# Optimization experiments

Measured on AMD Instinct MI355X. Metric: run time of the kernel, lower is better.

The kernel has to match this reference:

```python
import jax, jax.numpy as jnp
import numpy as np
import math

NUM_HEADS = 8
WINDOW = 8  # stage=1


def _windowed_attention(q, kv, Wq, bq, Wk, bk, Wv, bv, Wo, bo):
    B, N, C = q.shape
    H = W = int(math.isqrt(N))
    nh, ws = NUM_HEADS, WINDOW
    hd = C // nh
    scale = hd ** -0.5

    qp = q @ Wq + bq   # (B, N, C)
    kp = kv @ Wk + bk
    vp = kv @ Wv + bv

    def to_windows(x):
        # (B, N, C) -> (B, nh, nWh*nWw, ws*ws, hd)
        x = x.reshape(B, H // ws, ws, W // ws, ws, nh, hd)
        x = x.transpose(0, 5, 1, 3, 2, 4, 6)  # B, nh, nWh, nWw, ws, ws, hd
        return x.reshape(B, nh, (H // ws) * (W // ws), ws * ws, hd)

    qw = to_windows(qp)
    kw = to_windows(kp)
    vw = to_windows(vp)

    attn = jnp.einsum('bhnqd,bhnkd->bhnqk', qw, kw) * scale
    attn = jax.nn.softmax(attn.astype(jnp.float32), axis=-1).astype(qw.dtype)
    ow = jnp.einsum('bhnqk,bhnkd->bhnqd', attn, vw)

    # window reverse: (B, nh, nW, ws*ws, hd) -> (B, N, C)
    ow = ow.reshape(B, nh, H // ws, W // ws, ws, ws, hd)
    ow = ow.transpose(0, 2, 4, 3, 5, 1, 6)  # B, nWh, ws, nWw, ws, nh, hd
    x = ow.reshape(B, N, C)

    return x @ Wo + bo


def setup_inputs() -> dict:
    key = jax.random.key(0)
    ks = jax.random.split(key, 7)
    B, N, C = 4, 16384, 256
    s = 1.0 / math.sqrt(C)
    return {
        'q': jax.random.normal(ks[0], (B, N, C), jnp.float32),
        'kv': jax.random.normal(ks[1], (B, N, C), jnp.float32),
        'Wq': jax.random.normal(ks[2], (C, C), jnp.float32) * s,
        'bq': jnp.zeros((C,), jnp.float32),
        'Wk': jax.random.normal(ks[3], (C, C), jnp.float32) * s,
        'bk': jnp.zeros((C,), jnp.float32),
        'Wv': jax.random.normal(ks[4], (C, C), jnp.float32) * s,
        'bv': jnp.zeros((C,), jnp.float32),
        'Wo': jax.random.normal(ks[5], (C, C), jnp.float32) * s,
        'bo': jnp.zeros((C,), jnp.float32),
    }


def reference(q, kv, Wq, bq, Wk, bk, Wv, bv, Wo, bo):
    return _windowed_attention(q, kv, Wq, bq, Wk, bk, Wv, bv, Wo, bo)
```

## Files before the change

### kernel.cpp

```cpp
#include <hip/hip_runtime.h>
#include <hip/hip_bf16.h>

typedef __bf16 bf16;
typedef __bf16 bf16x8 __attribute__((ext_vector_type(8)));
typedef __bf16 bf16x4 __attribute__((ext_vector_type(4)));
typedef float  f32x4  __attribute__((ext_vector_type(4)));

#define DEVINL __device__ __forceinline__

DEVINL void gll16(const void* g, void* l) {
  __builtin_amdgcn_global_load_lds(
      (const __attribute__((address_space(1))) unsigned int*)g,
      (__attribute__((address_space(3))) unsigned int*)l, 16, 0, 0);
}

__global__ void k_prep(const float* __restrict__ Wq, const float* __restrict__ Wk,
                       const float* __restrict__ Wv, const float* __restrict__ Wo,
                       bf16* __restrict__ packQ, bf16* __restrict__ packO) {
  const int n = threadIdx.x;
  const int k = blockIdx.x;
  const int m = blockIdx.y;
  const int kk = k & 63, iter4 = k >> 6;
  const int h = kk >> 5, kg = (kk >> 3) & 3, e = k & 7;
  if (m < 3) {
    const float* W = (m == 0) ? Wq : (m == 1) ? Wk : Wv;
    const bf16 v = (bf16)W[k * 256 + n];
    const int nglob = m * 256 + n;
    const int tile = nglob >> 7, row = nglob & 127;
    const int kgs = kg ^ ((row >> 1) & 3);
    packQ[(size_t)((tile * 4 + iter4) * 1024 + h * 512 + row * 4 + kgs) * 8 + e] = v;
  } else {
    const float w = Wo[k * 256 + n];
    const bf16 hi = (bf16)w;
    const bf16 v = (m == 3) ? hi : (bf16)(w - (float)hi);
    const int iter = (m - 3) * 4 + iter4;
    const int tile = n >> 7, row = n & 127;
    const int kgs = kg ^ ((row >> 1) & 3);
    packO[(size_t)((tile * 8 + iter) * 1024 + h * 512 + row * 4 + kgs) * 8 + e] = v;
  }
}

__global__ __launch_bounds__(256, 3) void k_qkv(
    const float* __restrict__ q, const float* __restrict__ kv,
    const bf16* __restrict__ packQ,
    const float* __restrict__ bq, const float* __restrict__ bk,
    const float* __restrict__ bvv,
    bf16* __restrict__ qp, bf16* __restrict__ kp, bf16* __restrict__ vp) {
  __shared__ __align__(16) bf16 Bs[2][2][128 * 32];
  __shared__ __align__(16) bf16 Alds[128 * 64];

  const int g = blockIdx.x, xcd = g & 7, s = g >> 3;
  const int nb = s % 6, mh = s / 6;
  const int m0 = (mh * 8 + xcd) * 128;
  const float* A = (nb < 2) ? q : kv;

  const int tid = threadIdx.x, lane = tid & 63, wave = tid >> 6;
  const int lm = lane & 15, lq = lane >> 4;
  const int swzlq = lq ^ ((lm >> 1) & 3);
  const int mw = wave * 32;

  f32x4 acc[2][8];
#pragma unroll
  for (int t = 0; t < 2; ++t)
#pragma unroll
    for (int nf = 0; nf < 8; ++nf) acc[t][nf] = (f32x4)0.0f;

  const bf16* pbase = packQ + (size_t)nb * 4 * 8192;

  const int arow = tid >> 4;
  const int ac16 = tid & 15;
  float4 ar[8];

  auto loadA = [&](int it) {
#pragma unroll
    for (int u = 0; u < 8; ++u) {
      const int row = u * 16 + arow;
      ar[u] = *(const float4*)(A + (size_t)(m0 + row) * 256 + it * 64 + ac16 * 4);
    }
  };
  auto writeA = [&]() {
    const int gsl = ac16 >> 1, half = ac16 & 1;
#pragma unroll
    for (int u = 0; u < 8; ++u) {
      const int row = u * 16 + arow;
      const float4 f = ar[u];
      bf16x4 v;
      v[0] = (bf16)f.x; v[1] = (bf16)f.y; v[2] = (bf16)f.z; v[3] = (bf16)f.w;
      *(bf16x4*)&Alds[row * 64 + ((gsl ^ (row & 7)) << 3) + half * 4] = v;
    }
  };
  auto stageB = [&](int it, int buf) {
    const bf16* pit = pbase + it * 8192;
#pragma unroll
    for (int u = 0; u < 4; ++u) {
      const int c = u * 256 + tid;
      bf16* dst = (u < 2) ? &Bs[buf][0][c * 8] : &Bs[buf][1][(c - 512) * 8];
      gll16(pit + c * 8, dst);
    }
  };

  loadA(0);
  writeA();
  stageB(0, 0);
  __syncthreads();

#pragma unroll
  for (int i = 0; i < 4; ++i) {
    const int cur = i & 1;
    if (i < 3) {
      stageB(i + 1, cur ^ 1);
      loadA(i + 1);
    }
#pragma unroll
    for (int ks = 0; ks < 2; ++ks) {
      bf16x8 av[2], bvf[8];
#pragma unroll
      for (int t = 0; t < 2; ++t) {
        const int row = mw + t * 16 + lm;
        av[t] = *(const bf16x8*)&Alds[row * 64 + (((ks * 4 + lq) ^ (lm & 7)) << 3)];
      }
#pragma unroll
      for (int nf = 0; nf < 8; ++nf)
        bvf[nf] = *(const bf16x8*)&Bs[cur][ks][(nf * 16 + lm) * 32 + swzlq * 8];
#pragma unroll
      for (int t = 0; t < 2; ++t)
#pragma unroll
        for (int nf = 0; nf < 8; ++nf)
          acc[t][nf] = __builtin_amdgcn_mfma_f32_16x16x32_bf16(av[t], bvf[nf], acc[t][nf], 0, 0, 0);
    }
    if (i < 3) {
      __syncthreads();
      writeA();
      __syncthreads();
    }
  }

  const int ncbase = (nb * 128) & 255;
  bf16* op = (nb < 2) ? qp : (nb < 4) ? kp : vp;
  const float* bp = (nb < 2) ? bq : (nb < 4) ? bk : bvv;
#pragma unroll
  for (int t = 0; t < 2; ++t)
#pragma unroll
    for (int nf = 0; nf < 8; ++nf) {
      const int nc = ncbase + nf * 16 + lm;
      const float bval = bp[nc];
#pragma unroll
      for (int r = 0; r < 4; ++r) {
        const int mg = m0 + mw + t * 16 + lq * 4 + r;
        op[(size_t)mg * 256 + nc] = (bf16)(acc[t][nf][r] + bval);
      }
    }
}

__global__ __launch_bounds__(256, 3) void k_oproj(
    const bf16* __restrict__ ao, const bf16* __restrict__ packO,
    const float* __restrict__ bo, float* __restrict__ out) {
  __shared__ __align__(16) bf16 Bs[2][2][128 * 32];
  __shared__ __align__(16) bf16 Alds[128 * 64];

  const int g = blockIdx.x, xcd = g & 7, s = g >> 3;
  const int nb = s & 1, mh = s >> 1;
  const int m0 = (mh * 8 + xcd) * 128;

  const int tid = threadIdx.x, lane = tid & 63, wave = tid >> 6;
  const int lm = lane & 15, lq = lane >> 4;
  const int swzlq = lq ^ ((lm >> 1) & 3);
  const int mw = wave * 32;

  f32x4 acc[2][8];
#pragma unroll
  for (int t = 0; t < 2; ++t)
#pragma unroll
    for (int nf = 0; nf < 8; ++nf) acc[t][nf] = (f32x4)0.0f;

  const bf16* pbase = packO + (size_t)nb * 8 * 8192;

  const int arow = tid >> 3;
  const int ach  = tid & 7;
  bf16x8 arv[4];

  auto loadA = [&](int it) {
    const int kA = (it & 3) * 64;
#pragma unroll
    for (int u = 0; u < 4; ++u) {
      const int row = u * 32 + arow;
      arv[u] = *(const bf16x8*)(ao + (size_t)(m0 + row) * 256 + kA + ach * 8);
    }
  };
  auto writeA = [&]() {
#pragma unroll
    for (int u = 0; u < 4; ++u) {
      const int row = u * 32 + arow;
      *(bf16x8*)&Alds[row * 64 + ((ach ^ (row & 7)) << 3)] = arv[u];
    }
  };
  auto stageB = [&](int it, int buf) {
    const bf16* pit = pbase + (size_t)it * 8192;
#pragma unroll
    for (int u = 0; u < 4; ++u) {
      const int c = u * 256 + tid;
      bf16* dst = (u < 2) ? &Bs[buf][0][c * 8] : &Bs[buf][1][(c - 512) * 8];
      gll16(pit + c * 8, dst);
    }
  };

  loadA(0);
  writeA();
  stageB(0, 0);
  __syncthreads();

#pragma unroll
  for (int i = 0; i < 8; ++i) {
    const int cur = i & 1;
    if (i < 7) {
      stageB(i + 1, cur ^ 1);
      loadA(i + 1);
    }
#pragma unroll
    for (int ks = 0; ks < 2; ++ks) {
      bf16x8 av[2], bvf[8];
#pragma unroll
      for (int t = 0; t < 2; ++t) {
        const int row = mw + t * 16 + lm;
        av[t] = *(const bf16x8*)&Alds[row * 64 + (((ks * 4 + lq) ^ (lm & 7)) << 3)];
      }
#pragma unroll
      for (int nf = 0; nf < 8; ++nf)
        bvf[nf] = *(const bf16x8*)&Bs[cur][ks][(nf * 16 + lm) * 32 + swzlq * 8];
#pragma unroll
      for (int t = 0; t < 2; ++t)
#pragma unroll
        for (int nf = 0; nf < 8; ++nf)
          acc[t][nf] = __builtin_amdgcn_mfma_f32_16x16x32_bf16(av[t], bvf[nf], acc[t][nf], 0, 0, 0);
    }
    if (i < 7) {
      __syncthreads();
      writeA();
      __syncthreads();
    }
  }

#pragma unroll
  for (int t = 0; t < 2; ++t)
#pragma unroll
    for (int nf = 0; nf < 8; ++nf) {
      const int nglob = nb * 128 + nf * 16 + lm;
      const float bval = bo[nglob];
#pragma unroll
      for (int r = 0; r < 4; ++r) {
        const int mg = m0 + mw + t * 16 + lq * 4 + r;
        out[(size_t)mg * 256 + nglob] = acc[t][nf][r] + bval;
      }
    }
}

__global__ __launch_bounds__(256) void k_attn(
    const bf16* __restrict__ qp, const bf16* __restrict__ kp,
    const bf16* __restrict__ vp, bf16* __restrict__ ao) {
  __shared__ __align__(16) bf16 smem[3 * 64 * 136];
  bf16* Qs = smem;
  bf16* Ks = smem + 64 * 136;
  bf16* Vs = smem + 2 * 64 * 136;
  bf16* Ps = smem;
  bf16* Os = Vs;

  const int tid = threadIdx.x;
  const int lane = tid & 63;
  const int hl = tid >> 6;
  const int bw = blockIdx.x;
  const int b = bw >> 8;
  const int w = bw & 255;
  const int wy = w >> 4, wx = w & 15;
  const int ch0 = blockIdx.y * 128;

#pragma unroll
  for (int i = 0; i < 4; ++i) {
    const int c = i * 256 + tid;
    const int t = c >> 4;
    const int off = (c & 15) * 8;
    const int ty = t >> 3, tx = t & 7;
    const size_t gr = ((size_t)(b * 128 + wy * 8 + ty)) * 128 + wx * 8 + tx;
    const size_t gi = gr * 256 + ch0 + off;
    const int li = t * 136 + off;
    *(uint4*)&Qs[li] = *(const uint4*)&qp[gi];
    *(uint4*)&Ks[li] = *(const uint4*)&kp[gi];
    *(uint4*)&Vs[li] = *(const uint4*)&vp[gi];
  }
  __syncthreads();

  const int chh = hl * 32;
  const int lm = lane & 15;
  const int lq = lane >> 4;

  bf16x8 qa[4], kb[4];
#pragma unroll
  for (int t = 0; t < 4; ++t)
    qa[t] = *(const bf16x8*)&Qs[(t * 16 + lm) * 136 + chh + lq * 8];
#pragma unroll
  for (int t = 0; t < 4; ++t)
    kb[t] = *(const bf16x8*)&Ks[(t * 16 + lm) * 136 + chh + lq * 8];

  f32x4 s[4][4];
#pragma unroll
  for (int i = 0; i < 4; ++i)
#pragma unroll
    for (int j = 0; j < 4; ++j) s[i][j] = (f32x4)0.0f;
#pragma unroll
  for (int i = 0; i < 4; ++i)
#pragma unroll
    for (int j = 0; j < 4; ++j)
      s[i][j] = __builtin_amdgcn_mfma_f32_16x16x32_bf16(qa[i], kb[j], s[i][j], 0, 0, 0);

  const float scale = 0.17677669529663687f;
  float rl[4][4];
#pragma unroll
  for (int mt = 0; mt < 4; ++mt) {
#pragma unroll
    for (int r = 0; r < 4; ++r) {
      float mx = fmaxf(fmaxf(s[mt][0][r], s[mt][1][r]), fmaxf(s[mt][2][r], s[mt][3][r]));
      mx = fmaxf(mx, __shfl_xor(mx, 1));
      mx = fmaxf(mx, __shfl_xor(mx, 2));
      mx = fmaxf(mx, __shfl_xor(mx, 4));
      mx = fmaxf(mx, __shfl_xor(mx, 8));
      float sum = 0.f;
#pragma unroll
      for (int nt = 0; nt < 4; ++nt) {
        const float p = __expf((s[mt][nt][r] - mx) * scale);
        s[mt][nt][r] = p;
        sum += p;
      }
      sum += __shfl_xor(sum, 1);
      sum += __shfl_xor(sum, 2);
      sum += __shfl_xor(sum, 4);
      sum += __shfl_xor(sum, 8);
      rl[mt][r] = 1.0f / sum;
    }
  }

  __syncthreads();

  bf16* Ph = Ps + hl * 4096;
#pragma unroll
  for (int mt = 0; mt < 4; ++mt)
#pragma unroll
    for (int nt = 0; nt < 4; ++nt)
#pragma unroll
      for (int r = 0; r < 4; ++r) {
        const int qrow = mt * 16 + lq * 4 + r;
        const int kcol = nt * 16 + lm;
        Ph[qrow * 64 + (((kcol >> 3) ^ (qrow & 7)) << 3) + (kcol & 7)] = (bf16)s[mt][nt][r];
      }

  f32x4 o[4][2];
#pragma unroll
  for (int i = 0; i < 4; ++i) { o[i][0] = (f32x4)0.0f; o[i][1] = (f32x4)0.0f; }
#pragma unroll
  for (int ks = 0; ks < 2; ++ks) {
    bf16x8 pa[4];
#pragma unroll
    for (int mt = 0; mt < 4; ++mt) {
      const int qrow = mt * 16 + lm;
      const int gsel = ks * 4 + lq;
      pa[mt] = *(const bf16x8*)&Ph[qrow * 64 + ((gsel ^ (qrow & 7)) << 3)];
    }
    bf16x8 vbf[2];
#pragma unroll
    for (int ntd = 0; ntd < 2; ++ntd) {
      const int d = ntd * 16 + lm;
      bf16x8 tv;
#pragma unroll
      for (int j = 0; j < 8; ++j)
        tv[j] = Vs[(ks * 32 + lq * 8 + j) * 136 + chh + d];
      vbf[ntd] = tv;
    }
#pragma unroll
    for (int mt = 0; mt < 4; ++mt)
#pragma unroll
      for (int ntd = 0; ntd < 2; ++ntd)
        o[mt][ntd] = __builtin_amdgcn_mfma_f32_16x16x32_bf16(pa[mt], vbf[ntd], o[mt][ntd], 0, 0, 0);
  }

  __syncthreads();

#pragma unroll
  for (int mt = 0; mt < 4; ++mt)
#pragma unroll
    for (int ntd = 0; ntd < 2; ++ntd)
#pragma unroll
      for (int r = 0; r < 4; ++r) {
        const int qrow = mt * 16 + lq * 4 + r;
        const int d = ntd * 16 + lm;
        Os[qrow * 136 + chh + d] = (bf16)(o[mt][ntd][r] * rl[mt][r]);
      }
  __syncthreads();

#pragma unroll
  for (int i = 0; i < 4; ++i) {
    const int c = i * 256 + tid;
    const int t = c >> 4;
    const int off = (c & 15) * 8;
    const int ty = t >> 3, tx = t & 7;
    const size_t gr = ((size_t)(b * 128 + wy * 8 + ty)) * 128 + wx * 8 + tx;
    *(uint4*)&ao[gr * 256 + ch0 + off] = *(const uint4*)&Os[t * 136 + off];
  }
}

extern "C" void kernel_launch(void* const* d_in, const int* in_sizes, int n_in,
                              void* d_out, int out_size, void* d_ws, size_t ws_size,
                              hipStream_t stream) {
  const float* q  = (const float*)d_in[0];
  const float* kv = (const float*)d_in[1];
  const float* Wq = (const float*)d_in[2];
  const float* bq = (const float*)d_in[3];
  const float* Wk = (const float*)d_in[4];
  const float* bk = (const float*)d_in[5];
  const float* Wv = (const float*)d_in[6];
  const float* bv = (const float*)d_in[7];
  const float* Wo = (const float*)d_in[8];
  const float* bo = (const float*)d_in[9];
  float* out = (float*)d_out;

  char* ws = (char*)d_ws;
  bf16* packQ = (bf16*)(ws + 0);
  bf16* packO = (bf16*)(ws + 393216);
  const size_t PLANE = (size_t)65536 * 256 * 2;
  bf16* qp = (bf16*)(ws + 1048576);
  bf16* kp = (bf16*)(ws + 1048576 + PLANE);
  bf16* vp = (bf16*)(ws + 1048576 + 2 * PLANE);
  bf16* ao = (bf16*)(ws + 1048576 + 3 * PLANE);
  if (ws_size < 1048576 + 4 * PLANE) return;

  k_prep<<<dim3(256, 5), 256, 0, stream>>>(Wq, Wk, Wv, Wo, packQ, packO);
  k_qkv<<<3072, 256, 0, stream>>>(q, kv, packQ, bq, bk, bv, qp, kp, vp);
  k_attn<<<dim3(1024, 2), 256, 0, stream>>>(qp, kp, vp, ao);
  k_oproj<<<1024, 256, 0, stream>>>(ao, packO, bo, out);
}
```

Measured before the change: 288.0 us.

## Drop double buffering in projection GEMMs to raise occupancy to four blocks

The QKV and output-projection GEMM kernels go from double-buffered B tiles with register-prefetched A to a single LDS buffer. Each iteration now loads and writes its tile and then synchronizes before computing. This halves B shared memory and frees prefetch registers, so the launch bound rises from 3 to 4 blocks per CU. The cost is that global loads no longer overlap with MFMA work inside a block, so latency hiding relies on the extra resident blocks.

```diff
diff --git a/kernel.cpp b/kernel.cpp
--- a/kernel.cpp
+++ b/kernel.cpp
@@ -40,13 +40,13 @@
   }
 }
 
-__global__ __launch_bounds__(256, 3) void k_qkv(
+__global__ __launch_bounds__(256, 4) void k_qkv(
     const float* __restrict__ q, const float* __restrict__ kv,
     const bf16* __restrict__ packQ,
     const float* __restrict__ bq, const float* __restrict__ bk,
     const float* __restrict__ bvv,
     bf16* __restrict__ qp, bf16* __restrict__ kp, bf16* __restrict__ vp) {
-  __shared__ __align__(16) bf16 Bs[2][2][128 * 32];
+  __shared__ __align__(16) bf16 Bs[2][128 * 32];
   __shared__ __align__(16) bf16 Alds[128 * 64];
 
   const int g = blockIdx.x, xcd = g & 7, s = g >> 3;
@@ -89,28 +89,23 @@
       *(bf16x4*)&Alds[row * 64 + ((gsl ^ (row & 7)) << 3) + half * 4] = v;
     }
   };
-  auto stageB = [&](int it, int buf) {
+  auto stageB = [&](int it) {
     const bf16* pit = pbase + it * 8192;
 #pragma unroll
     for (int u = 0; u < 4; ++u) {
       const int c = u * 256 + tid;
-      bf16* dst = (u < 2) ? &Bs[buf][0][c * 8] : &Bs[buf][1][(c - 512) * 8];
+      bf16* dst = (u < 2) ? &Bs[0][c * 8] : &Bs[1][(c - 512) * 8];
       gll16(pit + c * 8, dst);
     }
   };
 
-  loadA(0);
-  writeA();
-  stageB(0, 0);
-  __syncthreads();
-
 #pragma unroll
   for (int i = 0; i < 4; ++i) {
-    const int cur = i & 1;
-    if (i < 3) {
-      stageB(i + 1, cur ^ 1);
-      loadA(i + 1);
-    }
+    if (i) __syncthreads();
+    stageB(i);
+    loadA(i);
+    writeA();
+    __syncthreads();
 #pragma unroll
     for (int ks = 0; ks < 2; ++ks) {
       bf16x8 av[2], bvf[8];
@@ -121,17 +116,12 @@
       }
 #pragma unroll
       for (int nf = 0; nf < 8; ++nf)
-        bvf[nf] = *(const bf16x8*)&Bs[cur][ks][(nf * 16 + lm) * 32 + swzlq * 8];
+        bvf[nf] = *(const bf16x8*)&Bs[ks][(nf * 16 + lm) * 32 + swzlq * 8];
 #pragma unroll
       for (int t = 0; t < 2; ++t)
 #pragma unroll
         for (int nf = 0; nf < 8; ++nf)
           acc[t][nf] = __builtin_amdgcn_mfma_f32_16x16x32_bf16(av[t], bvf[nf], acc[t][nf], 0, 0, 0);
-    }
-    if (i < 3) {
-      __syncthreads();
-      writeA();
-      __syncthreads();
     }
   }
 
@@ -152,10 +142,10 @@
     }
 }
 
-__global__ __launch_bounds__(256, 3) void k_oproj(
+__global__ __launch_bounds__(256, 4) void k_oproj(
     const bf16* __restrict__ ao, const bf16* __restrict__ packO,
     const float* __restrict__ bo, float* __restrict__ out) {
-  __shared__ __align__(16) bf16 Bs[2][2][128 * 32];
+  __shared__ __align__(16) bf16 Bs[2][128 * 32];
   __shared__ __align__(16) bf16 Alds[128 * 64];
 
   const int g = blockIdx.x, xcd = g & 7, s = g >> 3;
@@ -194,28 +184,23 @@
       *(bf16x8*)&Alds[row * 64 + ((ach ^ (row & 7)) << 3)] = arv[u];
     }
   };
-  auto stageB = [&](int it, int buf) {
+  auto stageB = [&](int it) {
     const bf16* pit = pbase + (size_t)it * 8192;
 #pragma unroll
     for (int u = 0; u < 4; ++u) {
       const int c = u * 256 + tid;
-      bf16* dst = (u < 2) ? &Bs[buf][0][c * 8] : &Bs[buf][1][(c - 512) * 8];
+      bf16* dst = (u < 2) ? &Bs[0][c * 8] : &Bs[1][(c - 512) * 8];
       gll16(pit + c * 8, dst);
     }
   };
 
-  loadA(0);
-  writeA();
-  stageB(0, 0);
-  __syncthreads();
-
 #pragma unroll
   for (int i = 0; i < 8; ++i) {
-    const int cur = i & 1;
-    if (i < 7) {
-      stageB(i + 1, cur ^ 1);
-      loadA(i + 1);
-    }
+    if (i) __syncthreads();
+    stageB(i);
+    loadA(i);
+    writeA();
+    __syncthreads();
 #pragma unroll
     for (int ks = 0; ks < 2; ++ks) {
       bf16x8 av[2], bvf[8];
@@ -226,17 +211,12 @@
       }
 #pragma unroll
       for (int nf = 0; nf < 8; ++nf)
-        bvf[nf] = *(const bf16x8*)&Bs[cur][ks][(nf * 16 + lm) * 32 + swzlq * 8];
+        bvf[nf] = *(const bf16x8*)&Bs[ks][(nf * 16 + lm) * 32 + swzlq * 8];
 #pragma unroll
       for (int t = 0; t < 2; ++t)
 #pragma unroll
         for (int nf = 0; nf < 8; ++nf)
           acc[t][nf] = __builtin_amdgcn_mfma_f32_16x16x32_bf16(av[t], bvf[nf], acc[t][nf], 0, 0, 0);
-    }
-    if (i < 7) {
-      __syncthreads();
-      writeA();
-      __syncthreads();
     }
   }
 
```

New measurement: 318.0 us. 1.1x slower.
